# Kernel tuning notes

Measured on AMD Instinct MI355X. Metric: run time of the kernel, lower is better.

The kernel has to match this reference:

```python
import jax, jax.numpy as jnp
import numpy as np

# TT-matrix embedding: vocab = 50*60*60 = 180000, embed_dim = 8*8*8 = 512, tt_rank = 16
M1, M2, M3 = 50, 60, 60        # row modes (index factorization)
N1, N2, N3 = 8, 8, 8           # col modes (embedding-dim factorization)
R = 16                         # TT rank
SENT, BATCH = 2048, 64
VOCAB = M1 * M2 * M3


def setup_inputs() -> dict:
    key = jax.random.key(0)
    k1, k2, k3, kx = jax.random.split(key, 4)
    scale = 0.3  # per-core stddev (t3.random_matrix uses a similar per-core normal init)
    # core k stored with the gathered (row-mode) axis first so gather is a plain take
    core1 = jax.random.normal(k1, (M1, N1, R), dtype=jnp.float32) * scale       # [m1, n1, r]
    core2 = jax.random.normal(k2, (M2, R, N2, R), dtype=jnp.float32) * scale    # [m2, r, n2, r]
    core3 = jax.random.normal(k3, (M3, R, N3), dtype=jnp.float32) * scale       # [m3, r, n3]
    x = jax.random.randint(kx, (SENT, BATCH), 0, VOCAB, dtype=jnp.int64)        # batch_dim_last=True layout
    return {"x": x, "core1": core1, "core2": core2, "core3": core3}


def reference(x, core1, core2, core3):
    # batch_dim_last=True: x is [sent, batch] -> permute to [batch, sent]
    sent, batch = x.shape
    flat = x.T.reshape(-1)                      # [T] flat token ids, T = batch*sent
    # t3.ind2sub: row-major mixed-radix decomposition over row modes [M1, M2, M3]
    i1 = flat // (M2 * M3)
    rem = flat % (M2 * M3)
    i2 = rem // M3
    i3 = rem % M3
    # gather one slice per TT core
    g1 = core1[i1]                              # [T, n1, r]
    g2 = core2[i2]                              # [T, r, n2, r]
    g3 = core3[i3]                              # [T, r, n3]
    # contract cores -> full embedding rows (t3.gather_rows(...).full())
    t12 = jnp.einsum('tar,trbs->tabs', g1, g2)  # [T, n1, n2, r]
    emb = jnp.einsum('tabs,tsc->tabc', t12, g3) # [T, n1, n2, n3]
    rows = emb.reshape(batch, sent, N1 * N2 * N3)
    # batch_dim_last=True: permute back to [sent, batch, emb_dim]
    return rows.transpose(1, 0, 2)
```

## Files before the change

kernel.cpp:

```cpp
#include <hip/hip_runtime.h>
#include <hip/hip_bf16.h>


#define M2M3 3600u
#define M3 60u

__global__ __launch_bounds__(256) void tt_pair_kernel(
    const float* __restrict__ c1,
    const float* __restrict__ c2,
    float* __restrict__ tab)
{
    const int pair = blockIdx.x;
    const int i1 = pair / 60;
    const int i2 = pair - i1 * 60;
    const int tid = threadIdx.x;
    const int q  = tid >> 6;
    const int ab = tid & 63;
    const int a  = ab >> 3;
    const int b  = ab & 7;

    const float* __restrict__ g1 = c1 + i1 * 128 + a * 16;
    const float* __restrict__ g2 = c2 + i2 * 2048 + b * 16 + q * 4;

    float4 acc = make_float4(0.f, 0.f, 0.f, 0.f);
#pragma unroll
    for (int r = 0; r < 16; ++r) {
        const float a1 = g1[r];
        const float4 v = *(const float4*)(g2 + r * 128);
        acc.x = fmaf(a1, v.x, acc.x);
        acc.y = fmaf(a1, v.y, acc.y);
        acc.z = fmaf(a1, v.z, acc.z);
        acc.w = fmaf(a1, v.w, acc.w);
    }
    *(float4*)(tab + (size_t)pair * 1024 + tid * 4) = acc;
}

__global__ __launch_bounds__(256) void tt_embed2_kernel(
    const int* __restrict__ x,
    const float* __restrict__ c3,
    const float* __restrict__ tab,
    float* __restrict__ out,
    int T)
{
    const int u    = (int)((blockIdx.x * blockDim.x + threadIdx.x) >> 6);
    const int lane = threadIdx.x & 63;
    if (u >= T) return;

    const unsigned id  = __builtin_amdgcn_readfirstlane((unsigned)x[u]);
    const unsigned i1  = id / M2M3;
    const unsigned rem = id - i1 * M2M3;
    const unsigned i2  = rem / M3;
    const unsigned i3  = rem - i2 * M3;

    const float* tp = tab + (size_t)(i1 * 60u + i2) * 1024u;
    float4 t[4];
#pragma unroll
    for (int q = 0; q < 4; ++q)
        t[q] = *(const float4*)(tp + q * 256 + lane * 4);
    const float* tf = (const float*)t;

    const float4* __restrict__ g3 = (const float4*)(c3 + i3 * 128u);

    float o[8];
#pragma unroll
    for (int c = 0; c < 8; ++c) o[c] = 0.f;

#pragma unroll
    for (int s = 0; s < 16; ++s) {
        const float ts = tf[s];
        const float4 w0 = g3[s * 2 + 0];
        const float4 w1 = g3[s * 2 + 1];
        o[0] = fmaf(ts, w0.x, o[0]);
        o[1] = fmaf(ts, w0.y, o[1]);
        o[2] = fmaf(ts, w0.z, o[2]);
        o[3] = fmaf(ts, w0.w, o[3]);
        o[4] = fmaf(ts, w1.x, o[4]);
        o[5] = fmaf(ts, w1.y, o[5]);
        o[6] = fmaf(ts, w1.z, o[6]);
        o[7] = fmaf(ts, w1.w, o[7]);
    }

    float4* dst = (float4*)(out + (size_t)u * 512 + lane * 8);
    dst[0] = make_float4(o[0], o[1], o[2], o[3]);
    dst[1] = make_float4(o[4], o[5], o[6], o[7]);
}

__global__ __launch_bounds__(256) void tt_embed_kernel(
    const int* __restrict__ x, const float* __restrict__ c1,
    const float* __restrict__ c2, const float* __restrict__ c3,
    float* __restrict__ out, int T)
{
    const int u    = (int)((blockIdx.x * blockDim.x + threadIdx.x) >> 6);
    const int lane = threadIdx.x & 63;
    if (u >= T) return;
    const int a = lane >> 3, b = lane & 7;
    const unsigned id  = (unsigned)x[u];
    const unsigned i1  = id / M2M3;
    const unsigned rem = id - i1 * M2M3;
    const unsigned i2  = rem / M3;
    const unsigned i3  = rem - i2 * M3;
    const float4* g1 = (const float4*)(c1 + i1 * 128u + a * 16);
    const float*  g2 = c2 + i2 * 2048u + b * 16;
    const float4* g3 = (const float4*)(c3 + i3 * 128u);
    float4 a1v[4];
#pragma unroll
    for (int q = 0; q < 4; ++q) a1v[q] = g1[q];
    const float* a1f = (const float*)a1v;
    float t12[16];
#pragma unroll
    for (int s = 0; s < 16; ++s) t12[s] = 0.f;
#pragma unroll
    for (int r = 0; r < 16; ++r) {
        const float a1 = a1f[r];
        const float4* row = (const float4*)(g2 + r * 128);
#pragma unroll
        for (int q = 0; q < 4; ++q) {
            const float4 v = row[q];
            t12[q*4+0] = fmaf(a1, v.x, t12[q*4+0]);
            t12[q*4+1] = fmaf(a1, v.y, t12[q*4+1]);
            t12[q*4+2] = fmaf(a1, v.z, t12[q*4+2]);
            t12[q*4+3] = fmaf(a1, v.w, t12[q*4+3]);
        }
    }
    float o[8];
#pragma unroll
    for (int c = 0; c < 8; ++c) o[c] = 0.f;
#pragma unroll
    for (int s = 0; s < 16; ++s) {
        const float ts = t12[s];
        const float4 w0 = g3[s*2+0];
        const float4 w1 = g3[s*2+1];
        o[0]=fmaf(ts,w0.x,o[0]); o[1]=fmaf(ts,w0.y,o[1]);
        o[2]=fmaf(ts,w0.z,o[2]); o[3]=fmaf(ts,w0.w,o[3]);
        o[4]=fmaf(ts,w1.x,o[4]); o[5]=fmaf(ts,w1.y,o[5]);
        o[6]=fmaf(ts,w1.z,o[6]); o[7]=fmaf(ts,w1.w,o[7]);
    }
    float4* dst = (float4*)(out + (size_t)u * 512 + lane * 8);
    dst[0] = make_float4(o[0], o[1], o[2], o[3]);
    dst[1] = make_float4(o[4], o[5], o[6], o[7]);
}

extern "C" void kernel_launch(void* const* d_in, const int* in_sizes, int n_in,
                              void* d_out, int out_size, void* d_ws, size_t ws_size,
                              hipStream_t stream) {
    const int*   x  = (const int*)d_in[0];
    const float* c1 = (const float*)d_in[1];
    const float* c2 = (const float*)d_in[2];
    const float* c3 = (const float*)d_in[3];
    float* out = (float*)d_out;

    const int T = in_sizes[0];
    const size_t tab_bytes = 3000u * 1024u * sizeof(float);

    if (ws_size >= tab_bytes) {
        float* tab = (float*)d_ws;
        tt_pair_kernel<<<3000, 256, 0, stream>>>(c1, c2, tab);
        const int blocks = (T + 3) / 4;
        tt_embed2_kernel<<<blocks, 256, 0, stream>>>(x, c3, tab, out, T);
    } else {
        const int blocks = (T + 3) / 4;
        tt_embed_kernel<<<blocks, 256, 0, stream>>>(x, c1, c2, c3, out, T);
    }
}
```

Baseline: 335.8 us.

## Bucket tokens by (i1,i2) pair and compute per-pair embeddings in place

Drops the precomputed 12MB pair table. Instead it builds a counting sort of tokens by their (i1,i2) pair: zero, histogram, scan, then an atomic scatter into a permutation. Each block then computes its pair's t12 product in registers and emits output rows for every token in that bucket. This removes the table write and its reads, but adds four extra launches plus atomics. It also scatters output writes in non-contiguous token order.

```diff
diff --git a/kernel.cpp b/kernel.cpp
--- a/kernel.cpp
+++ b/kernel.cpp
@@ -4,85 +4,128 @@
 
 #define M2M3 3600u
 #define M3 60u
-
-__global__ __launch_bounds__(256) void tt_pair_kernel(
+#define NPAIR 3000
+#define EMB_BLOCK 256
+
+__global__ __launch_bounds__(256) void tt_zero_kernel(int* __restrict__ counts) {
+    const int i = blockIdx.x * blockDim.x + threadIdx.x;
+    if (i < NPAIR) counts[i] = 0;
+}
+
+__global__ __launch_bounds__(256) void tt_hist_kernel(
+    const int* __restrict__ x, int* __restrict__ counts, int T)
+{
+    const int u = blockIdx.x * blockDim.x + threadIdx.x;
+    if (u >= T) return;
+    const unsigned pair = (unsigned)x[u] / M3;
+    atomicAdd(&counts[pair], 1);
+}
+
+__global__ __launch_bounds__(1024) void tt_scan_kernel(
+    const int* __restrict__ counts, int* __restrict__ bases, int* __restrict__ cursors)
+{
+    __shared__ int s[1024];
+    const int t = threadIdx.x;
+    const int c0 = t * 3;
+    const int v0 = (c0     < NPAIR) ? counts[c0]     : 0;
+    const int v1 = (c0 + 1 < NPAIR) ? counts[c0 + 1] : 0;
+    const int v2 = (c0 + 2 < NPAIR) ? counts[c0 + 2] : 0;
+    const int mysum = v0 + v1 + v2;
+    s[t] = mysum;
+    __syncthreads();
+    for (int off = 1; off < 1024; off <<= 1) {
+        int val = (t >= off) ? s[t - off] : 0;
+        __syncthreads();
+        if (t >= off) s[t] += val;
+        __syncthreads();
+    }
+    int excl = s[t] - mysum;
+    if (c0 < NPAIR)     { bases[c0]     = excl; cursors[c0]     = excl; }
+    excl += v0;
+    if (c0 + 1 < NPAIR) { bases[c0 + 1] = excl; cursors[c0 + 1] = excl; }
+    excl += v1;
+    if (c0 + 2 < NPAIR) { bases[c0 + 2] = excl; cursors[c0 + 2] = excl; }
+}
+
+__global__ __launch_bounds__(256) void tt_scatter_kernel(
+    const int* __restrict__ x, int* __restrict__ cursors,
+    int* __restrict__ perm, int T)
+{
+    const int u = blockIdx.x * blockDim.x + threadIdx.x;
+    if (u >= T) return;
+    const unsigned pair = (unsigned)x[u] / M3;
+    const int pos = atomicAdd(&cursors[pair], 1);
+    perm[pos] = u;
+}
+
+__global__ __launch_bounds__(256) void tt_bucket_embed_kernel(
+    const int* __restrict__ x,
     const float* __restrict__ c1,
     const float* __restrict__ c2,
-    float* __restrict__ tab)
+    const float* __restrict__ c3,
+    const int* __restrict__ bases,
+    const int* __restrict__ counts,
+    const int* __restrict__ perm,
+    float* __restrict__ out)
 {
     const int pair = blockIdx.x;
     const int i1 = pair / 60;
     const int i2 = pair - i1 * 60;
-    const int tid = threadIdx.x;
-    const int q  = tid >> 6;
-    const int ab = tid & 63;
-    const int a  = ab >> 3;
-    const int b  = ab & 7;
+    const int wave = threadIdx.x >> 6;
+    const int lane = threadIdx.x & 63;
+    const int a = lane >> 3;
+    const int b = lane & 7;
+
+    const int base  = bases[pair];
+    const int count = counts[pair];
+    if (count == 0) return;
 
     const float* __restrict__ g1 = c1 + i1 * 128 + a * 16;
-    const float* __restrict__ g2 = c2 + i2 * 2048 + b * 16 + q * 4;
-
-    float4 acc = make_float4(0.f, 0.f, 0.f, 0.f);
+    const float* __restrict__ g2 = c2 + i2 * 2048 + b * 16;
+    float t12[16];
+#pragma unroll
+    for (int s = 0; s < 16; ++s) t12[s] = 0.f;
 #pragma unroll
     for (int r = 0; r < 16; ++r) {
         const float a1 = g1[r];
-        const float4 v = *(const float4*)(g2 + r * 128);
-        acc.x = fmaf(a1, v.x, acc.x);
-        acc.y = fmaf(a1, v.y, acc.y);
-        acc.z = fmaf(a1, v.z, acc.z);
-        acc.w = fmaf(a1, v.w, acc.w);
-    }
-    *(float4*)(tab + (size_t)pair * 1024 + tid * 4) = acc;
-}
-
-__global__ __launch_bounds__(256) void tt_embed2_kernel(
-    const int* __restrict__ x,
-    const float* __restrict__ c3,
-    const float* __restrict__ tab,
-    float* __restrict__ out,
-    int T)
-{
-    const int u    = (int)((blockIdx.x * blockDim.x + threadIdx.x) >> 6);
-    const int lane = threadIdx.x & 63;
-    if (u >= T) return;
-
-    const unsigned id  = __builtin_amdgcn_readfirstlane((unsigned)x[u]);
-    const unsigned i1  = id / M2M3;
-    const unsigned rem = id - i1 * M2M3;
-    const unsigned i2  = rem / M3;
-    const unsigned i3  = rem - i2 * M3;
-
-    const float* tp = tab + (size_t)(i1 * 60u + i2) * 1024u;
-    float4 t[4];
-#pragma unroll
-    for (int q = 0; q < 4; ++q)
-        t[q] = *(const float4*)(tp + q * 256 + lane * 4);
-    const float* tf = (const float*)t;
-
-    const float4* __restrict__ g3 = (const float4*)(c3 + i3 * 128u);
-
-    float o[8];
-#pragma unroll
-    for (int c = 0; c < 8; ++c) o[c] = 0.f;
-
-#pragma unroll
-    for (int s = 0; s < 16; ++s) {
-        const float ts = tf[s];
-        const float4 w0 = g3[s * 2 + 0];
-        const float4 w1 = g3[s * 2 + 1];
-        o[0] = fmaf(ts, w0.x, o[0]);
-        o[1] = fmaf(ts, w0.y, o[1]);
-        o[2] = fmaf(ts, w0.z, o[2]);
-        o[3] = fmaf(ts, w0.w, o[3]);
-        o[4] = fmaf(ts, w1.x, o[4]);
-        o[5] = fmaf(ts, w1.y, o[5]);
-        o[6] = fmaf(ts, w1.z, o[6]);
-        o[7] = fmaf(ts, w1.w, o[7]);
-    }
-
-    float4* dst = (float4*)(out + (size_t)u * 512 + lane * 8);
-    dst[0] = make_float4(o[0], o[1], o[2], o[3]);
-    dst[1] = make_float4(o[4], o[5], o[6], o[7]);
+        const float4* row = (const float4*)(g2 + r * 128);
+#pragma unroll
+        for (int q = 0; q < 4; ++q) {
+            const float4 v = row[q];
+            t12[q * 4 + 0] = fmaf(a1, v.x, t12[q * 4 + 0]);
+            t12[q * 4 + 1] = fmaf(a1, v.y, t12[q * 4 + 1]);
+            t12[q * 4 + 2] = fmaf(a1, v.z, t12[q * 4 + 2]);
+            t12[q * 4 + 3] = fmaf(a1, v.w, t12[q * 4 + 3]);
+        }
+    }
+
+    for (int k = wave; k < count; k += 4) {
+        const int u = __builtin_amdgcn_readfirstlane(perm[base + k]);
+        const unsigned id = __builtin_amdgcn_readfirstlane((unsigned)x[u]);
+        const unsigned i3 = id % M3;
+        const float4* __restrict__ g3 = (const float4*)(c3 + i3 * 128u);
+
+        float o[8];
+#pragma unroll
+        for (int c = 0; c < 8; ++c) o[c] = 0.f;
+#pragma unroll
+        for (int s = 0; s < 16; ++s) {
+            const float ts = t12[s];
+            const float4 w0 = g3[s * 2 + 0];
+            const float4 w1 = g3[s * 2 + 1];
+            o[0] = fmaf(ts, w0.x, o[0]);
+            o[1] = fmaf(ts, w0.y, o[1]);
+            o[2] = fmaf(ts, w0.z, o[2]);
+            o[3] = fmaf(ts, w0.w, o[3]);
+            o[4] = fmaf(ts, w1.x, o[4]);
+            o[5] = fmaf(ts, w1.y, o[5]);
+            o[6] = fmaf(ts, w1.z, o[6]);
+            o[7] = fmaf(ts, w1.w, o[7]);
+        }
+        float4* dst = (float4*)(out + (size_t)u * 512 + lane * 8);
+        dst[0] = make_float4(o[0], o[1], o[2], o[3]);
+        dst[1] = make_float4(o[4], o[5], o[6], o[7]);
+    }
 }
 
 __global__ __launch_bounds__(256) void tt_embed_kernel(
@@ -150,13 +193,21 @@
     float* out = (float*)d_out;
 
     const int T = in_sizes[0];
-    const size_t tab_bytes = 3000u * 1024u * sizeof(float);
-
-    if (ws_size >= tab_bytes) {
-        float* tab = (float*)d_ws;
-        tt_pair_kernel<<<3000, 256, 0, stream>>>(c1, c2, tab);
-        const int blocks = (T + 3) / 4;
-        tt_embed2_kernel<<<blocks, 256, 0, stream>>>(x, c3, tab, out, T);
+
+    const size_t need = (size_t)(3 * NPAIR + T) * sizeof(int);
+
+    if (ws_size >= need) {
+        int* counts  = (int*)d_ws;
+        int* bases   = counts + NPAIR;
+        int* cursors = bases + NPAIR;
+        int* perm    = cursors + NPAIR;
+
+        tt_zero_kernel<<<(NPAIR + 255) / 256, 256, 0, stream>>>(counts);
+        tt_hist_kernel<<<(T + 255) / 256, 256, 0, stream>>>(x, counts, T);
+        tt_scan_kernel<<<1, 1024, 0, stream>>>(counts, bases, cursors);
+        tt_scatter_kernel<<<(T + 255) / 256, 256, 0, stream>>>(x, cursors, perm, T);
+        tt_bucket_embed_kernel<<<NPAIR, EMB_BLOCK, 0, stream>>>(
+            x, c1, c2, c3, bases, counts, perm, out);
     } else {
         const int blocks = (T + 3) / 4;
         tt_embed_kernel<<<blocks, 256, 0, stream>>>(x, c1, c2, c3, out, T);
```

Result: no change. 336.6 us (+0.2%).
